# Kernel optimization log

Measured on AMD Instinct MI355X. Metric: run time of the kernel, lower is better.

## Reference

```python
import jax, jax.numpy as jnp
import numpy as np

B, T, D = 32, 400, 64
EPS = 1e-6


def setup_inputs() -> dict:
    key = jax.random.key(0)
    k1, k2, k3 = jax.random.split(key, 3)
    x = jax.random.normal(k1, (B, T, D), dtype=jnp.float32)
    mu = jax.random.normal(k2, (B, T, D), dtype=jnp.float32)
    # Build SPD covariance matrices: A A^T / D + I
    A = jax.random.normal(k3, (B, T, D, D), dtype=jnp.float32)
    sigma = jnp.einsum('btij,btkj->btik', A, A) / D + jnp.eye(D, dtype=jnp.float32)
    return {"x": x, "mu": mu, "sigma": sigma}


def reference(x, mu, sigma):
    d = sigma.shape[-1]
    # Regularize and factorize: sigma + eps*I = L L^T
    L = jnp.linalg.cholesky(sigma + EPS * jnp.eye(d, dtype=sigma.dtype))  # [B,T,D,D]
    diff = x - mu  # [B,T,D]
    # Solve L z = diff (batched lower-triangular solve)
    z = jax.scipy.linalg.solve_triangular(L, diff[..., None], lower=True)[..., 0]  # [B,T,D]
    log_det = jnp.sum(jnp.log(jnp.diagonal(L, axis1=-2, axis2=-1)), axis=-1)  # [B,T]
    log_prob = -0.5 * jnp.sum(z * z, axis=-1) - log_det - 0.5 * d * jnp.log(2.0 * jnp.pi)
    ll = jnp.mean(jnp.sum(log_prob, axis=1), axis=0)  # sum over time, mean over batch
    return jnp.expand_dims(-ll, axis=-1)  # shape [1]
```

## Files before the change

kernel.cpp:

```cpp
#include <hip/hip_runtime.h>

#define D_   64
#define NBT_ 12800
#define B_   32

__device__ __forceinline__ float rl(float v, int l) {
    return __uint_as_float(__builtin_amdgcn_readlane(__float_as_uint(v), l));
}

__global__ __launch_bounds__(256) void chol_ll(const float* __restrict__ x,
                                               const float* __restrict__ mu,
                                               const float* __restrict__ sigma,
                                               float* __restrict__ partial) {
    const int lane = threadIdx.x & 63;
    const int wv   = threadIdx.x >> 6;
    const int bt   = blockIdx.x * 4 + wv;

    const float4* srow = (const float4*)(sigma + (size_t)bt * (D_ * D_) + (size_t)lane * D_);
    float row[D_];
    #pragma unroll
    for (int m = 0; m < D_ / 4; ++m) {
        float4 t = srow[m];
        row[4 * m + 0] = t.x; row[4 * m + 1] = t.y;
        row[4 * m + 2] = t.z; row[4 * m + 3] = t.w;
    }
    float d = x[bt * D_ + lane] - mu[bt * D_ + lane];

    float q = 0.f, lg = 0.f;
    #pragma unroll
    for (int k = 0; k < D_; ++k) {
        float s   = rl(row[k], k) + 1e-6f;
        float inv = __builtin_amdgcn_rsqf(s);
        lg += __builtin_amdgcn_logf(s);
        row[k] *= inv;
        float zk = rl(d, k) * inv;
        q += zk * zk;
        d -= row[k] * zk;
        #pragma unroll
        for (int j = k + 1; j < D_; ++j)
            row[j] -= row[k] * rl(row[k], j);
    }
    if (lane == 0) {
        float log_det = 0.34657359027997264f * lg;
        float lp = -0.5f * q - log_det - 58.81206612509905f;
        partial[bt] = lp;
    }
}

__global__ __launch_bounds__(1024) void reduce_ll(const float* __restrict__ partial,
                                                  float* __restrict__ out) {
    float s = 0.f;
    for (int i = threadIdx.x; i < NBT_; i += 1024) s += partial[i];
    #pragma unroll
    for (int off = 32; off > 0; off >>= 1) s += __shfl_down(s, off, 64);
    __shared__ float ws[16];
    const int lane = threadIdx.x & 63, w = threadIdx.x >> 6;
    if (lane == 0) ws[w] = s;
    __syncthreads();
    if (threadIdx.x == 0) {
        float t = 0.f;
        #pragma unroll
        for (int i = 0; i < 16; ++i) t += ws[i];
        out[0] = -t / (float)B_;
    }
}

extern "C" void kernel_launch(void* const* d_in, const int* in_sizes, int n_in,
                              void* d_out, int out_size, void* d_ws, size_t ws_size,
                              hipStream_t stream) {
    const float* x     = (const float*)d_in[0];
    const float* mu    = (const float*)d_in[1];
    const float* sigma = (const float*)d_in[2];
    float* partial = (float*)d_ws;
    chol_ll<<<NBT_ / 4, 256, 0, stream>>>(x, mu, sigma, partial);
    reduce_ll<<<1, 1024, 0, stream>>>(partial, (float*)d_out);
}
```

Measured before the change: 338.8 us.

## Block Cholesky into 16-column panels staged through LDS to cut register pressure

Replaces the 64-register per-lane row with a left-looking blocked Cholesky over four 16-column panels. Finished panels are written to shared memory and read back to update later panels, so each lane keeps only 16 live values plus a temporary. This lowers VGPR usage and should raise occupancy and latency hiding for the sigma loads, at the cost of extra LDS traffic and readlane work for the panel updates.

Result: slower. 357.9 us (+5.6%).

```diff
diff --git a/kernel.cpp b/kernel.cpp
--- a/kernel.cpp
+++ b/kernel.cpp
@@ -1,6 +1,7 @@
 #include <hip/hip_runtime.h>
 
 #define D_   64
+#define CH   16
 #define NBT_ 12800
 #define B_   32
 
@@ -12,34 +13,57 @@
                                                const float* __restrict__ mu,
                                                const float* __restrict__ sigma,
                                                float* __restrict__ partial) {
+    __shared__ float lds[4][3][CH][D_];
     const int lane = threadIdx.x & 63;
     const int wv   = threadIdx.x >> 6;
     const int bt   = blockIdx.x * 4 + wv;
 
-    const float4* srow = (const float4*)(sigma + (size_t)bt * (D_ * D_) + (size_t)lane * D_);
-    float row[D_];
+    const float* base = sigma + (size_t)bt * (D_ * D_) + (size_t)lane * D_;
+    float d = x[bt * D_ + lane] - mu[bt * D_ + lane];
+    float q = 0.f, lg = 0.f;
+
     #pragma unroll
-    for (int m = 0; m < D_ / 4; ++m) {
-        float4 t = srow[m];
-        row[4 * m + 0] = t.x; row[4 * m + 1] = t.y;
-        row[4 * m + 2] = t.z; row[4 * m + 3] = t.w;
+    for (int t = 0; t < 4; ++t) {
+        float cur[CH];
+        const float4* p = (const float4*)(base + t * CH);
+        #pragma unroll
+        for (int r = 0; r < 4; ++r) {
+            float4 v = p[r];
+            cur[4 * r + 0] = v.x; cur[4 * r + 1] = v.y;
+            cur[4 * r + 2] = v.z; cur[4 * r + 3] = v.w;
+        }
+        #pragma unroll
+        for (int m = 0; m < t; ++m) {
+            float tmp[CH];
+            #pragma unroll
+            for (int k = 0; k < CH; ++k) tmp[k] = lds[wv][m][k][lane];
+            #pragma unroll
+            for (int k = 0; k < CH; ++k) {
+                #pragma unroll
+                for (int c = 0; c < CH; ++c)
+                    cur[c] = __builtin_fmaf(-tmp[k], rl(tmp[k], t * CH + c), cur[c]);
+            }
+        }
+        #pragma unroll
+        for (int kk = 0; kk < CH; ++kk) {
+            const int gk = t * CH + kk;
+            float s   = rl(cur[kk], gk) + 1e-6f;
+            float inv = __builtin_amdgcn_rsqf(s);
+            lg += __builtin_amdgcn_logf(s);
+            cur[kk] *= inv;
+            float zk = rl(d, gk) * inv;
+            q += zk * zk;
+            d = __builtin_fmaf(-cur[kk], zk, d);
+            #pragma unroll
+            for (int c = kk + 1; c < CH; ++c)
+                cur[c] = __builtin_fmaf(-cur[kk], rl(cur[kk], t * CH + c), cur[c]);
+        }
+        if (t < 3) {
+            #pragma unroll
+            for (int c = 0; c < CH; ++c) lds[wv][t][c][lane] = cur[c];
+        }
     }
-    float d = x[bt * D_ + lane] - mu[bt * D_ + lane];
 
-    float q = 0.f, lg = 0.f;
-    #pragma unroll
-    for (int k = 0; k < D_; ++k) {
-        float s   = rl(row[k], k) + 1e-6f;
-        float inv = __builtin_amdgcn_rsqf(s);
-        lg += __builtin_amdgcn_logf(s);
-        row[k] *= inv;
-        float zk = rl(d, k) * inv;
-        q += zk * zk;
-        d -= row[k] * zk;
-        #pragma unroll
-        for (int j = k + 1; j < D_; ++j)
-            row[j] -= row[k] * rl(row[k], j);
-    }
     if (lane == 0) {
         float log_det = 0.34657359027997264f * lg;
         float lp = -0.5f * q - log_det - 58.81206612509905f;
```
